# Performance work log

Measured on AMD Instinct MI355X. Metric: run time of the kernel, lower is better.

## Reference

```python
import jax, jax.numpy as jnp
import numpy as np

N = 50000      # nodes
E = 800000     # edges (before self-loops)
F_IN = 128     # node feature dim (= hidden)
HID = 128      # hidden
H = 4          # heads
C = HID // H   # per-head channels = 32
L = 4          # conv_feat + 3 GATLayers
G = 128        # graphs in batch
EPS = 1e-5
BN_BIAS = 1e-4


def setup_inputs() -> dict:
    key = jax.random.key(0)
    ks = jax.random.split(key, 12)
    s = 0.1
    x = jax.random.normal(ks[0], (N, F_IN), jnp.float32)
    edge_index = jax.random.randint(ks[1], (2, E), 0, N)
    batch = jnp.sort(jax.random.randint(ks[2], (N,), 0, G))
    gat_lin = jax.random.normal(ks[3], (L, HID, HID), jnp.float32) * s
    att_src = jax.random.normal(ks[4], (L, H, C), jnp.float32) * s
    att_dst = jax.random.normal(ks[5], (L, H, C), jnp.float32) * s
    gat_bias = jax.random.normal(ks[6], (L, HID), jnp.float32) * s
    fc_w = jax.random.normal(ks[7], (HID, HID), jnp.float32) * s
    fc_b = jax.random.normal(ks[8], (HID,), jnp.float32) * s
    cls_w = jax.random.normal(ks[9], (HID, 2), jnp.float32) * s
    cls_b = jax.random.normal(ks[10], (2,), jnp.float32) * s
    return {"x": x, "edge_index": edge_index, "batch": batch,
            "gat_lin": gat_lin, "att_src": att_src, "att_dst": att_dst,
            "gat_bias": gat_bias, "fc_w": fc_w, "fc_b": fc_b,
            "cls_w": cls_w, "cls_b": cls_b}


def batch_norm(h):
    # training-mode BN, weight=1, bias=1e-4 (per ResGAT init loop)
    m = h.mean(axis=0)
    v = h.var(axis=0)
    return (h - m) * jax.lax.rsqrt(v + EPS) + BN_BIAS


def gat_conv(x, W, a_src, a_dst, b, src, dst):
    # PyG GATConv: h = xW -> [N,H,C]; alpha_e = leaky_relu(a_src.h[src] + a_dst.h[dst]);
    # softmax over edges sharing the same dst; out[dst] += alpha * h[src]; concat heads + bias
    n = x.shape[0]
    h = (x @ W).reshape(n, H, C)
    a_s = jnp.einsum('nhc,hc->nh', h, a_src)   # [N,H]
    a_d = jnp.einsum('nhc,hc->nh', h, a_dst)   # [N,H]
    alpha = jax.nn.leaky_relu(a_s[src] + a_d[dst], 0.2)  # [E',H]
    amax = jax.lax.stop_gradient(jax.ops.segment_max(alpha, dst, num_segments=n))
    ealpha = jnp.exp(alpha - amax[dst])
    denom = jax.ops.segment_sum(ealpha, dst, num_segments=n)
    coef = ealpha / (denom[dst] + 1e-16)                 # [E',H]
    msg = h[src] * coef[:, :, None]                      # [E',H,C]
    out = jax.ops.segment_sum(msg, dst, num_segments=n)  # [N,H,C]
    return out.reshape(n, H * C) + b


def reference(x, edge_index, batch, gat_lin, att_src, att_dst, gat_bias,
              fc_w, fc_b, cls_w, cls_b):
    n = x.shape[0]
    loop = jnp.arange(n, dtype=edge_index.dtype)
    src = jnp.concatenate([edge_index[0], loop])  # add self-loops (PyG default)
    dst = jnp.concatenate([edge_index[1], loop])

    h = batch_norm(x)
    h = jax.nn.relu(gat_conv(h, gat_lin[0], att_src[0], att_dst[0], gat_bias[0], src, dst))
    for i in range(1, L):  # 3 GATLayers: relu(BN(GAT(h)) + h)
        out = gat_conv(h, gat_lin[i], att_src[i], att_dst[i], gat_bias[i], src, dst)
        h = jax.nn.relu(batch_norm(out) + h)

    g = jax.ops.segment_sum(h, batch, num_segments=G)  # global_add_pool [G,HID]
    g = jax.nn.relu(batch_norm(g) @ fc_w + fc_b)       # single FC layer (num_fc_layers=2)
    g = batch_norm(g)                                  # bn_hidden; dropout = identity (eval)
    logits = g @ cls_w + cls_b
    return jax.nn.log_softmax(logits, axis=-1)
```

## Files before the change

kernel.cpp:

```cpp
#include <hip/hip_runtime.h>
#include <math.h>

#define NF 128
#define EPS 1e-5f
#define BNB 1e-4f
#define CHUNK 8192

static inline int cdiv(int a, int b){ return (a + b - 1) / b; }

typedef __attribute__((ext_vector_type(8))) short bf16x8;
typedef __attribute__((ext_vector_type(4))) float f32x4;

__device__ __forceinline__ float lrelu(float x){ return x > 0.f ? x : 0.2f * x; }
__device__ __forceinline__ float sel4(float4 v, int h){
  float r = v.x;
  r = (h == 1) ? v.y : r;
  r = (h == 2) ? v.z : r;
  r = (h == 3) ? v.w : r;
  return r;
}

__device__ __forceinline__ unsigned short f2b(float f){
  unsigned u = __float_as_uint(f);
  u += 0x7fffu + ((u >> 16) & 1u);
  return (unsigned short)(u >> 16);
}
__device__ __forceinline__ float b2f_lo(unsigned v){ return __uint_as_float(v << 16); }
__device__ __forceinline__ float b2f_hi(unsigned v){ return __uint_as_float(v & 0xffff0000u); }

__global__ __launch_bounds__(256) void k_init(float* stats, int* bcnt, int nbkt, int statcount,
                                              const float* __restrict__ W,
                                              unsigned short* __restrict__ Wt){
  int i = blockIdx.x * blockDim.x + threadIdx.x;
  if (i < statcount) stats[i] = 0.f;
  if (i < nbkt) bcnt[i] = 0;
  int l = i >> 14, rem = i & 16383;
  int k = rem >> 7, nn = rem & 127;
  Wt[(l << 14) + nn * 128 + k] = f2b(W[i]);
}

__global__ __launch_bounds__(256) void k_bhist(const int* __restrict__ ei, int E, int n,
                                               int* __restrict__ bcnt, int nbkt){
  __shared__ int h[256];
  h[threadIdx.x] = 0;
  __syncthreads();
  int total = E + n;
  for (int i = blockIdx.x * 256 + threadIdx.x; i < total; i += gridDim.x * 256){
    int d = (i < E) ? ei[E + i] : (i - E);
    atomicAdd(&h[d >> 8], 1);
  }
  __syncthreads();
  if (threadIdx.x < nbkt && h[threadIdx.x]) atomicAdd(&bcnt[threadIdx.x], h[threadIdx.x]);
}

__global__ __launch_bounds__(256) void k_bscan(const int* __restrict__ bcnt, int* __restrict__ boff,
                                               int* __restrict__ bcursor, int nb){
  int t = threadIdx.x;
  int v = (t < nb) ? bcnt[t] : 0;
  int lane = t & 63, w = t >> 6;
  int x = v;
  #pragma unroll
  for (int d = 1; d < 64; d <<= 1){
    int y = __shfl_up(x, d, 64);
    if (lane >= d) x += y;
  }
  __shared__ int wt[4], wex[4];
  if (lane == 63) wt[w] = x;
  __syncthreads();
  if (t == 0){ int r = 0; for (int i = 0; i < 4; ++i){ wex[i] = r; r += wt[i]; } }
  __syncthreads();
  int ex = wex[w] + x - v;
  if (t < nb){ boff[t] = ex; bcursor[t] = ex; }
  if (t == nb - 1) boff[nb] = ex + v;
}

__global__ __launch_bounds__(256) void k_bscatter2(const int* __restrict__ ei, int E, int n,
                                                   int* __restrict__ bcursor,
                                                   unsigned* __restrict__ ebuf, int nbkt){
  __shared__ int h[256], base[256];
  int t = threadIdx.x;
  int total = E + n;
  int lo = blockIdx.x * CHUNK;
  int hi = min(lo + CHUNK, total);
  h[t] = 0;
  __syncthreads();
  for (int i = lo + t; i < hi; i += 256){
    int d = (i < E) ? ei[E + i] : (i - E);
    atomicAdd(&h[d >> 8], 1);
  }
  __syncthreads();
  int cnt = h[t];
  if (t < nbkt && cnt > 0) base[t] = atomicAdd(&bcursor[t], cnt);
  __syncthreads();
  h[t] = 0;
  __syncthreads();
  for (int i = lo + t; i < hi; i += 256){
    int s, d;
    if (i < E){ s = ei[i]; d = ei[E + i]; }
    else { s = i - E; d = s; }
    int b = d >> 8;
    int r = atomicAdd(&h[b], 1);
    ebuf[base[b] + r] = ((unsigned)s << 8) | (unsigned)(d & 255);
  }
}

__global__ __launch_bounds__(256) void k_bucket(const unsigned* __restrict__ ebuf,
                                                const int* __restrict__ boff,
                                                int* __restrict__ off,
                                                int* __restrict__ esrc, int n){
  __shared__ int h[256], sbase[256];
  __shared__ int wt[4], wex[4];
  int t = threadIdx.x, b = blockIdx.x;
  int lo = boff[b], hi = boff[b + 1];
  h[t] = 0;
  __syncthreads();
  for (int i = lo + t; i < hi; i += 256) atomicAdd(&h[ebuf[i] & 255u], 1);
  __syncthreads();
  int v = h[t];
  int lane = t & 63, w = t >> 6;
  int x = v;
  #pragma unroll
  for (int d = 1; d < 64; d <<= 1){
    int y = __shfl_up(x, d, 64);
    if (lane >= d) x += y;
  }
  if (lane == 63) wt[w] = x;
  __syncthreads();
  if (t == 0){ int r = 0; for (int i = 0; i < 4; ++i){ wex[i] = r; r += wt[i]; } }
  __syncthreads();
  int base = lo + wex[w] + (x - v);
  int node = b * 256 + t;
  if (node < n) off[node] = base;
  if (node == n - 1) off[n] = base + v;
  sbase[t] = base;
  __syncthreads();
  h[t] = 0;
  __syncthreads();
  for (int i = lo + t; i < hi; i += 256){
    unsigned pk = ebuf[i];
    int ld = (int)(pk & 255u);
    int s  = (int)(pk >> 8);
    int r = atomicAdd(&h[ld], 1);
    esrc[sbase[ld] + r] = s;
  }
}

__global__ __launch_bounds__(256) void k_colstats(const float* __restrict__ X, int n, float* __restrict__ out){
  __shared__ float ss[4][128], sq[4][128];
  int t = threadIdx.x, lane = t & 63, w = t >> 6;
  float sx = 0.f, sy = 0.f, qx = 0.f, qy = 0.f;
  for (int r = blockIdx.x * 4 + w; r < n; r += gridDim.x * 4){
    float2 v = *(const float2*)(X + (size_t)r * NF + lane * 2);
    sx += v.x; sy += v.y; qx += v.x * v.x; qy += v.y * v.y;
  }
  ss[w][lane * 2] = sx; ss[w][lane * 2 + 1] = sy;
  sq[w][lane * 2] = qx; sq[w][lane * 2 + 1] = qy;
  __syncthreads();
  if (t < 128){
    float tot = ss[0][t] + ss[1][t] + ss[2][t] + ss[3][t];
    atomicAdd(&out[t], tot);
  } else {
    int c = t - 128;
    float tot = sq[0][c] + sq[1][c] + sq[2][c] + sq[3][c];
    atomicAdd(&out[128 + c], tot);
  }
}

__global__ void k_bnx(const float* __restrict__ X, const float* __restrict__ stats,
                      float* __restrict__ H, ushort4* __restrict__ H16, int n){
  size_t tot4 = (size_t)n * (NF / 4);
  float inv_n = 1.f / (float)n;
  for (size_t i = blockIdx.x * (size_t)blockDim.x + threadIdx.x; i < tot4;
       i += (size_t)gridDim.x * blockDim.x){
    float4 v = ((const float4*)X)[i];
    int c0 = (int)((i * 4) % NF);
    float* vv = (float*)&v;
    #pragma unroll
    for (int j = 0; j < 4; ++j){
      float m = stats[c0 + j] * inv_n;
      float var = stats[128 + c0 + j] * inv_n - m * m;
      vv[j] = (vv[j] - m) * rsqrtf(var + EPS) + BNB;
    }
    ((float4*)H)[i] = v;
    ushort4 b;
    b.x = f2b(v.x); b.y = f2b(v.y); b.z = f2b(v.z); b.w = f2b(v.w);
    H16[i] = b;
  }
}

__global__ void k_bnres(const float* __restrict__ Xg, const float* __restrict__ stats,
                        float* __restrict__ H, ushort4* __restrict__ H16, int n){
  size_t tot4 = (size_t)n * (NF / 4);
  float inv_n = 1.f / (float)n;
  for (size_t i = blockIdx.x * (size_t)blockDim.x + threadIdx.x; i < tot4;
       i += (size_t)gridDim.x * blockDim.x){
    float4 v = ((const float4*)Xg)[i];
    float4 hc = ((const float4*)H)[i];
    int c0 = (int)((i * 4) % NF);
    float* vv = (float*)&v;
    float* hh = (float*)&hc;
    #pragma unroll
    for (int j = 0; j < 4; ++j){
      float m = stats[c0 + j] * inv_n;
      float var = stats[128 + c0 + j] * inv_n - m * m;
      float z = (vv[j] - m) * rsqrtf(var + EPS) + BNB + hh[j];
      hh[j] = fmaxf(z, 0.f);
    }
    ((float4*)H)[i] = hc;
    ushort4 b;
    b.x = f2b(hc.x); b.y = f2b(hc.y); b.z = f2b(hc.z); b.w = f2b(hc.w);
    H16[i] = b;
  }
}

__global__ __launch_bounds__(512) void k_gemm(const unsigned short* __restrict__ X,
                                              const unsigned short* __restrict__ Wt,
                                              unsigned short* __restrict__ Y,
                                              const float* __restrict__ asrc,
                                              const float* __restrict__ adst,
                                              float* __restrict__ a_s,
                                              float* __restrict__ a_d, int n){
  __shared__ unsigned short sX[128 * 128];
  __shared__ unsigned short sW[128 * 128];
  int t = threadIdx.x;
  int rbase = blockIdx.x * 128;
  #pragma unroll
  for (int i = 0; i < 4; ++i){
    int idx = t + 512 * i;
    int rn = idx >> 4, c16 = idx & 15;
    uint4 v = ((const uint4*)Wt)[idx];
    *(uint4*)&sW[rn * 128 + ((c16 ^ (rn & 7)) << 3)] = v;
  }
  #pragma unroll
  for (int i = 0; i < 4; ++i){
    int idx = t + 512 * i;
    int r = idx >> 4, c16 = idx & 15;
    int gr = rbase + r;
    uint4 v = (gr < n) ? ((const uint4*)(X + (size_t)gr * NF))[c16] : make_uint4(0, 0, 0, 0);
    *(uint4*)&sX[r * 128 + ((c16 ^ (r & 7)) << 3)] = v;
  }
  __syncthreads();
  int lane = t & 63, w = t >> 6;
  int lrow = w * 16 + (lane & 15);
  int khi = lane >> 4;
  bf16x8 a[4];
  #pragma unroll
  for (int ks = 0; ks < 4; ++ks){
    int c16 = ks * 4 + khi;
    a[ks] = *(const bf16x8*)&sX[lrow * 128 + ((c16 ^ (lrow & 7)) << 3)];
  }
  f32x4 acc[8];
  #pragma unroll
  for (int nt = 0; nt < 8; ++nt){
    f32x4 z = {0.f, 0.f, 0.f, 0.f};
    acc[nt] = z;
    int nrow = nt * 16 + (lane & 15);
    #pragma unroll
    for (int ks = 0; ks < 4; ++ks){
      int c16 = ks * 4 + khi;
      bf16x8 b = *(const bf16x8*)&sW[nrow * 128 + ((c16 ^ (nrow & 7)) << 3)];
      acc[nt] = __builtin_amdgcn_mfma_f32_16x16x32_bf16(a[ks], b, acc[nt], 0, 0, 0);
    }
  }
  #pragma unroll
  for (int nt = 0; nt < 8; ++nt){
    #pragma unroll
    for (int i = 0; i < 4; ++i){
      int r = w * 16 + (khi << 2) + i;
      int c = nt * 16 + (lane & 15);
      int csw = c ^ ((r & 7) << 3);
      sX[r * 128 + csw] = f2b(acc[nt][i]);
    }
  }
  __syncthreads();
  #pragma unroll
  for (int i = 0; i < 4; ++i){
    int idx = t + 512 * i;
    int r = idx >> 4, c16 = idx & 15;
    int gr = rbase + r;
    if (gr < n)
      ((uint4*)(Y + (size_t)gr * NF))[c16] = *(const uint4*)&sX[r * 128 + ((c16 ^ (r & 7)) << 3)];
  }
  int r = t >> 2, hh = t & 3;
  int gr = rbase + r;
  if (gr < n){
    float ps = 0.f, pd = 0.f;
    #pragma unroll
    for (int j = 0; j < 16; ++j){
      int c = hh * 32 + j * 2;
      int u = (c >> 3) ^ (r & 7);
      unsigned v = *(const unsigned*)&sX[r * 128 + (u << 3) + (c & 7)];
      float vx = b2f_lo(v), vy = b2f_hi(v);
      ps += vx * asrc[c] + vy * asrc[c + 1];
      pd += vx * adst[c] + vy * adst[c + 1];
    }
    a_s[(size_t)gr * 4 + hh] = ps;
    a_d[(size_t)gr * 4 + hh] = pd;
  }
}

__global__ __launch_bounds__(256) void k_attn(const unsigned short* __restrict__ Hm16,
                                              const float* __restrict__ a_s,
                                              const float* __restrict__ a_d,
                                              const int* __restrict__ off,
                                              const int* __restrict__ esrc,
                                              const float* __restrict__ bias,
                                              float* __restrict__ Yf,
                                              unsigned short* __restrict__ Y16,
                                              int dorelu, int n){
  int t = threadIdx.x, lane = t & 63, w = t >> 6;
  int node = blockIdx.x * 4 + w;
  if (node >= n) return;
  node = __builtin_amdgcn_readfirstlane(node);
  int head = lane >> 4;
  float4 ad4 = ((const float4*)a_d)[node];
  float adh = sel4(ad4, head);
  int lo = off[node], hi = off[node + 1];
  lo = __builtin_amdgcn_readfirstlane(lo);
  hi = __builtin_amdgcn_readfirstlane(hi);
  int fo = lane * 2;
  float sum = 0.f, ax = 0.f, ay = 0.f;
  for (int e = lo; e < hi; e += 8){
    int si[8]; float ai[8]; unsigned vi[8];
    #pragma unroll
    for (int k = 0; k < 8; ++k) si[k] = esrc[min(e + k, hi - 1)];
    #pragma unroll
    for (int k = 0; k < 8; ++k) ai[k] = a_s[(si[k] << 2) + head];
    #pragma unroll
    for (int k = 0; k < 8; ++k) vi[k] = *(const unsigned*)(Hm16 + (size_t)si[k] * NF + fo);
    #pragma unroll
    for (int k = 0; k < 8; ++k){
      float wgt = (e + k < hi) ? __expf(lrelu(ai[k] + adh)) : 0.f;
      sum += wgt;
      ax += wgt * b2f_lo(vi[k]);
      ay += wgt * b2f_hi(vi[k]);
    }
  }
  float inv = 1.f / (sum + 1e-16f);
  float2 b = *(const float2*)(bias + fo);
  float rx = ax * inv + b.x;
  float ry = ay * inv + b.y;
  if (dorelu){
    rx = fmaxf(rx, 0.f); ry = fmaxf(ry, 0.f);
    ushort2 pk; pk.x = f2b(rx); pk.y = f2b(ry);
    *(ushort2*)(Y16 + (size_t)node * NF + fo) = pk;
  }
  float2 r; r.x = rx; r.y = ry;
  *(float2*)(Yf + (size_t)node * NF + fo) = r;
}

__global__ __launch_bounds__(256) void k_pool(const float* __restrict__ H, const int* __restrict__ batch,
                                              float* __restrict__ g, int n){
  int gid = blockIdx.x;
  int t = threadIdx.x, lane = t & 63, w = t >> 6;
  int lo = 0, hi = n;
  while (lo < hi){ int mid = (lo + hi) >> 1; if (batch[mid] < gid) lo = mid + 1; else hi = mid; }
  int a = lo, b = n;
  while (a < b){ int mid = (a + b) >> 1; if (batch[mid] < gid + 1) a = mid + 1; else b = mid; }
  float sx = 0.f, sy = 0.f;
  for (int r = lo + w; r < a; r += 4){
    float2 v = *(const float2*)(H + (size_t)r * NF + lane * 2);
    sx += v.x; sy += v.y;
  }
  __shared__ float ss[4][128];
  ss[w][lane * 2] = sx; ss[w][lane * 2 + 1] = sy;
  __syncthreads();
  if (t < 128) g[(size_t)gid * NF + t] = ss[0][t] + ss[1][t] + ss[2][t] + ss[3][t];
}

__global__ __launch_bounds__(256) void k_h2(const float* __restrict__ g,
                                            const float* __restrict__ st1,
                                            const float* __restrict__ fc_w,
                                            const float* __restrict__ fc_b,
                                            float* __restrict__ hfc,
                                            float* __restrict__ st2){
  __shared__ float sA[32 * 128];
  __shared__ float sW[128 * 128];
  __shared__ float redS[8][128], redQ[8][128];
  int t = threadIdx.x;
  int rbase = blockIdx.x * 32;
  #pragma unroll
  for (int i = 0; i < 16; ++i)
    ((float4*)sW)[t + 256 * i] = ((const float4*)fc_w)[t + 256 * i];
  const float inv128 = 1.f / 128.f;
  #pragma unroll
  for (int i = 0; i < 4; ++i){
    int idx = t + 256 * i;
    int r = idx >> 5, c4 = idx & 31;
    float4 v = ((const float4*)(g + (size_t)(rbase + r) * 128))[c4];
    int c0 = c4 * 4;
    float* vv = (float*)&v;
    #pragma unroll
    for (int j = 0; j < 4; ++j){
      float m = st1[c0 + j] * inv128;
      float var = st1[128 + c0 + j] * inv128 - m * m;
      vv[j] = (vv[j] - m) * rsqrtf(var + EPS) + BNB;
    }
    ((float4*)sA)[idx] = v;
  }
  __syncthreads();
  int c0 = (t & 31) * 4, r0 = (t >> 5) * 4;
  float o[4][4];
  float4 bb = *(const float4*)(fc_b + c0);
  #pragma unroll
  for (int i = 0; i < 4; ++i){ o[i][0] = bb.x; o[i][1] = bb.y; o[i][2] = bb.z; o[i][3] = bb.w; }
  for (int k = 0; k < 128; ++k){
    float4 wv = *(const float4*)&sW[k * 128 + c0];
    #pragma unroll
    for (int i = 0; i < 4; ++i){
      float xs = sA[(r0 + i) * 128 + k];
      o[i][0] += xs * wv.x; o[i][1] += xs * wv.y;
      o[i][2] += xs * wv.z; o[i][3] += xs * wv.w;
    }
  }
  float ps[4] = {0, 0, 0, 0}, pq[4] = {0, 0, 0, 0};
  #pragma unroll
  for (int i = 0; i < 4; ++i){
    #pragma unroll
    for (int j = 0; j < 4; ++j){
      float v = fmaxf(o[i][j], 0.f);
      o[i][j] = v;
      ps[j] += v; pq[j] += v * v;
    }
    float4 wv; wv.x = o[i][0]; wv.y = o[i][1]; wv.z = o[i][2]; wv.w = o[i][3];
    *(float4*)(hfc + (size_t)(rbase + r0 + i) * 128 + c0) = wv;
  }
  int g8 = t >> 5;
  #pragma unroll
  for (int j = 0; j < 4; ++j){ redS[g8][c0 + j] = ps[j]; redQ[g8][c0 + j] = pq[j]; }
  __syncthreads();
  if (t < 128){
    float s = 0.f, q = 0.f;
    #pragma unroll
    for (int gg = 0; gg < 8; ++gg){ s += redS[gg][t]; q += redQ[gg][t]; }
    atomicAdd(&st2[t], s);
    atomicAdd(&st2[128 + t], q);
  }
}

__global__ __launch_bounds__(1024) void k_h3(const float* __restrict__ hfc,
                                             const float* __restrict__ st2,
                                             const float* __restrict__ cls_w,
                                             const float* __restrict__ cls_b,
                                             float* __restrict__ out){
  __shared__ float A[128 * 128];
  __shared__ float logits[256];
  int t = threadIdx.x;
  #pragma unroll
  for (int i = 0; i < 4; ++i)
    ((float4*)A)[t + 1024 * i] = ((const float4*)hfc)[t + 1024 * i];
  __syncthreads();
  const float inv128 = 1.f / 128.f;
  #pragma unroll
  for (int i = 0; i < 16; ++i){
    int idx = t + 1024 * i;
    int c = idx & 127;
    float m = st2[c] * inv128;
    float var = st2[128 + c] * inv128 - m * m;
    A[idx] = (A[idx] - m) * rsqrtf(var + EPS) + BNB;
  }
  __syncthreads();
  int o = t >> 2, sub = t & 3;
  int r = o >> 1, j = o & 1;
  float acc = 0.f;
  int k0 = sub * 32;
  for (int k = k0; k < k0 + 32; ++k)
    acc += A[r * 128 + k] * cls_w[k * 2 + j];
  acc += __shfl_xor(acc, 1, 64);
  acc += __shfl_xor(acc, 2, 64);
  if (sub == 0) logits[o] = acc + cls_b[j];
  __syncthreads();
  if (t < 256){
    int rr = t >> 1;
    float l0 = logits[rr * 2], l1 = logits[rr * 2 + 1];
    float mx = fmaxf(l0, l1);
    float lse = mx + logf(__expf(l0 - mx) + __expf(l1 - mx));
    out[t] = logits[t] - lse;
  }
}

extern "C" void kernel_launch(void* const* d_in, const int* in_sizes, int n_in,
                              void* d_out, int out_size, void* d_ws, size_t ws_size,
                              hipStream_t stream){
  const float* x        = (const float*)d_in[0];
  const int*   ei       = (const int*)d_in[1];
  const int*   batch    = (const int*)d_in[2];
  const float* gat_lin  = (const float*)d_in[3];
  const float* att_src  = (const float*)d_in[4];
  const float* att_dst  = (const float*)d_in[5];
  const float* gat_bias = (const float*)d_in[6];
  const float* fc_w     = (const float*)d_in[7];
  const float* fc_b     = (const float*)d_in[8];
  const float* cls_w    = (const float*)d_in[9];
  const float* cls_b    = (const float*)d_in[10];
  float* out = (float*)d_out;
  (void)n_in; (void)out_size; (void)ws_size;

  int N = in_sizes[0] / NF;
  int E = in_sizes[1] / 2;
  int total = E + N;
  int nbkt = cdiv(N, 256);

  char* p = (char*)d_ws;
  auto alloc = [&](size_t bytes) -> char* {
    char* r = p;
    p += (bytes + 255) & ~(size_t)255;
    return r;
  };
  int*   off     = (int*)alloc((size_t)(N + 1) * 4);
  int*   bcnt    = (int*)alloc((size_t)nbkt * 4);
  int*   boff    = (int*)alloc((size_t)(nbkt + 1) * 4);
  int*   bcursor = (int*)alloc((size_t)nbkt * 4);
  unsigned* ebuf = (unsigned*)alloc((size_t)total * 4);
  int*   esrc    = (int*)alloc((size_t)total * 4);
  float* stats   = (float*)alloc(8 * 256 * 4);
  float* hbuf    = (float*)alloc((size_t)N * NF * 4);
  unsigned short* hbuf16 = (unsigned short*)alloc((size_t)N * NF * 2);
  unsigned short* tmp16  = (unsigned short*)alloc((size_t)N * NF * 2);
  unsigned short* wbuf16 = (unsigned short*)alloc((size_t)4 * NF * NF * 2);
  float* gout    = (float*)alloc((size_t)N * NF * 4);
  float* a_s     = (float*)alloc((size_t)N * 4 * 4);
  float* a_d     = (float*)alloc((size_t)N * 4 * 4);
  float* gpool   = (float*)alloc(128 * NF * 4);
  float* hfc     = (float*)alloc(128 * NF * 4);

  k_init<<<256, 256, 0, stream>>>(stats, bcnt, nbkt, 1536, gat_lin, wbuf16);
  k_bhist<<<256, 256, 0, stream>>>(ei, E, N, bcnt, nbkt);
  k_bscan<<<1, 256, 0, stream>>>(bcnt, boff, bcursor, nbkt);
  k_bscatter2<<<cdiv(total, CHUNK), 256, 0, stream>>>(ei, E, N, bcursor, ebuf, nbkt);
  k_bucket<<<nbkt, 256, 0, stream>>>(ebuf, boff, off, esrc, N);

  k_colstats<<<256, 256, 0, stream>>>(x, N, stats);
  k_bnx<<<1024, 256, 0, stream>>>(x, stats, hbuf, (ushort4*)hbuf16, N);

  for (int L = 0; L < 4; ++L){
    k_gemm<<<cdiv(N, 128), 512, 0, stream>>>(hbuf16, wbuf16 + (size_t)L * NF * NF, tmp16,
                                             att_src + (size_t)L * NF, att_dst + (size_t)L * NF,
                                             a_s, a_d, N);
    if (L == 0){
      k_attn<<<cdiv(N, 4), 256, 0, stream>>>(tmp16, a_s, a_d, off, esrc,
                                             gat_bias + (size_t)L * NF,
                                             hbuf, hbuf16, 1, N);
    } else {
      k_attn<<<cdiv(N, 4), 256, 0, stream>>>(tmp16, a_s, a_d, off, esrc,
                                             gat_bias + (size_t)L * NF,
                                             gout, hbuf16, 0, N);
      k_colstats<<<256, 256, 0, stream>>>(gout, N, stats + L * 256);
      k_bnres<<<1024, 256, 0, stream>>>(gout, stats + L * 256, hbuf, (ushort4*)hbuf16, N);
    }
  }

  k_pool<<<128, 256, 0, stream>>>(hbuf, batch, gpool, N);
  k_colstats<<<32, 256, 0, stream>>>(gpool, 128, stats + 1024);
  k_h2<<<4, 256, 0, stream>>>(gpool, stats + 1024, fc_w, fc_b, hfc, stats + 1280);
  k_h3<<<1, 1024, 0, stream>>>(hfc, stats + 1280, cls_w, cls_b, out);
}
```

Measured before the change: 453.9 us.

## Fuse batch-norm and residual into GEMM prologue and pooling, use exp2

Removes the standalone BN-on-input and BN+residual+ReLU kernels. Normalization is now applied while the GEMM loads its A tile: mode 1 is plain BN, mode 2 is BN plus residual plus ReLU, and mode 2 also writes the updated fp32 residual. The final layer's BN/residual/ReLU is folded into the pooling kernel. Attention logits are prescaled by log2(e) so the edge softmax can use exp2f. This drops several full passes over the node-feature arrays, at the cost of a heavier GEMM prologue and recomputing the per-column statistics in every block.

After: 433.6 us. 1.05x faster.

```diff
diff --git a/kernel.cpp b/kernel.cpp
--- a/kernel.cpp
+++ b/kernel.cpp
@@ -5,6 +5,7 @@
 #define EPS 1e-5f
 #define BNB 1e-4f
 #define CHUNK 8192
+#define LOG2E 1.44269504088896f
 
 static inline int cdiv(int a, int b){ return (a + b - 1) / b; }
 
@@ -24,6 +25,9 @@
   unsigned u = __float_as_uint(f);
   u += 0x7fffu + ((u >> 16) & 1u);
   return (unsigned short)(u >> 16);
+}
+__device__ __forceinline__ unsigned pack2(float a, float b){
+  return (unsigned)f2b(a) | ((unsigned)f2b(b) << 16);
 }
 __device__ __forceinline__ float b2f_lo(unsigned v){ return __uint_as_float(v << 16); }
 __device__ __forceinline__ float b2f_hi(unsigned v){ return __uint_as_float(v & 0xffff0000u); }
@@ -166,54 +170,11 @@
   }
 }
 
-__global__ void k_bnx(const float* __restrict__ X, const float* __restrict__ stats,
-                      float* __restrict__ H, ushort4* __restrict__ H16, int n){
-  size_t tot4 = (size_t)n * (NF / 4);
-  float inv_n = 1.f / (float)n;
-  for (size_t i = blockIdx.x * (size_t)blockDim.x + threadIdx.x; i < tot4;
-       i += (size_t)gridDim.x * blockDim.x){
-    float4 v = ((const float4*)X)[i];
-    int c0 = (int)((i * 4) % NF);
-    float* vv = (float*)&v;
-    #pragma unroll
-    for (int j = 0; j < 4; ++j){
-      float m = stats[c0 + j] * inv_n;
-      float var = stats[128 + c0 + j] * inv_n - m * m;
-      vv[j] = (vv[j] - m) * rsqrtf(var + EPS) + BNB;
-    }
-    ((float4*)H)[i] = v;
-    ushort4 b;
-    b.x = f2b(v.x); b.y = f2b(v.y); b.z = f2b(v.z); b.w = f2b(v.w);
-    H16[i] = b;
-  }
-}
-
-__global__ void k_bnres(const float* __restrict__ Xg, const float* __restrict__ stats,
-                        float* __restrict__ H, ushort4* __restrict__ H16, int n){
-  size_t tot4 = (size_t)n * (NF / 4);
-  float inv_n = 1.f / (float)n;
-  for (size_t i = blockIdx.x * (size_t)blockDim.x + threadIdx.x; i < tot4;
-       i += (size_t)gridDim.x * blockDim.x){
-    float4 v = ((const float4*)Xg)[i];
-    float4 hc = ((const float4*)H)[i];
-    int c0 = (int)((i * 4) % NF);
-    float* vv = (float*)&v;
-    float* hh = (float*)&hc;
-    #pragma unroll
-    for (int j = 0; j < 4; ++j){
-      float m = stats[c0 + j] * inv_n;
-      float var = stats[128 + c0 + j] * inv_n - m * m;
-      float z = (vv[j] - m) * rsqrtf(var + EPS) + BNB + hh[j];
-      hh[j] = fmaxf(z, 0.f);
-    }
-    ((float4*)H)[i] = hc;
-    ushort4 b;
-    b.x = f2b(hc.x); b.y = f2b(hc.y); b.z = f2b(hc.z); b.w = f2b(hc.w);
-    H16[i] = b;
-  }
-}
-
-__global__ __launch_bounds__(512) void k_gemm(const unsigned short* __restrict__ X,
+__global__ __launch_bounds__(512) void k_gemm(const unsigned short* __restrict__ X16,
+                                              const float* __restrict__ Xa,
+                                              float* __restrict__ Xb,
+                                              const float* __restrict__ stats, float inv_n,
+                                              int mode,
                                               const unsigned short* __restrict__ Wt,
                                               unsigned short* __restrict__ Y,
                                               const float* __restrict__ asrc,
@@ -231,13 +192,66 @@
     uint4 v = ((const uint4*)Wt)[idx];
     *(uint4*)&sW[rn * 128 + ((c16 ^ (rn & 7)) << 3)] = v;
   }
-  #pragma unroll
-  for (int i = 0; i < 4; ++i){
-    int idx = t + 512 * i;
-    int r = idx >> 4, c16 = idx & 15;
-    int gr = rbase + r;
-    uint4 v = (gr < n) ? ((const uint4*)(X + (size_t)gr * NF))[c16] : make_uint4(0, 0, 0, 0);
-    *(uint4*)&sX[r * 128 + ((c16 ^ (r & 7)) << 3)] = v;
+  if (mode == 0){
+    #pragma unroll
+    for (int i = 0; i < 4; ++i){
+      int idx = t + 512 * i;
+      int r = idx >> 4, c16 = idx & 15;
+      int gr = rbase + r;
+      uint4 v = (gr < n) ? ((const uint4*)(X16 + (size_t)gr * NF))[c16] : make_uint4(0, 0, 0, 0);
+      *(uint4*)&sX[r * 128 + ((c16 ^ (r & 7)) << 3)] = v;
+    }
+  } else {
+    #pragma unroll
+    for (int i = 0; i < 4; ++i){
+      int idx = t + 512 * i;
+      int r = idx >> 4, c16 = idx & 15;
+      int gr = rbase + r;
+      int c = c16 * 8;
+      float z[8];
+      if (gr < n){
+        float4 va = *(const float4*)(Xa + (size_t)gr * NF + c);
+        float4 vb = *(const float4*)(Xa + (size_t)gr * NF + c + 4);
+        float4 m1 = *(const float4*)(stats + c);
+        float4 m2 = *(const float4*)(stats + c + 4);
+        float4 q1 = *(const float4*)(stats + 128 + c);
+        float4 q2 = *(const float4*)(stats + 128 + c + 4);
+        const float* pa = (const float*)&va; const float* pb = (const float*)&vb;
+        const float* pm1 = (const float*)&m1; const float* pm2 = (const float*)&m2;
+        const float* pq1 = (const float*)&q1; const float* pq2 = (const float*)&q2;
+        #pragma unroll
+        for (int j = 0; j < 4; ++j){
+          float m = pm1[j] * inv_n;
+          float var = pq1[j] * inv_n - m * m;
+          z[j] = (pa[j] - m) * rsqrtf(var + EPS) + BNB;
+          float m_ = pm2[j] * inv_n;
+          float var_ = pq2[j] * inv_n - m_ * m_;
+          z[4 + j] = (pb[j] - m_) * rsqrtf(var_ + EPS) + BNB;
+        }
+        if (mode == 2){
+          float4 ha = *(const float4*)(Xb + (size_t)gr * NF + c);
+          float4 hb = *(const float4*)(Xb + (size_t)gr * NF + c + 4);
+          const float* ph1 = (const float*)&ha; const float* ph2 = (const float*)&hb;
+          #pragma unroll
+          for (int j = 0; j < 4; ++j){
+            z[j]     = fmaxf(z[j]     + ph1[j], 0.f);
+            z[4 + j] = fmaxf(z[4 + j] + ph2[j], 0.f);
+          }
+          float4 o1, o2;
+          o1.x = z[0]; o1.y = z[1]; o1.z = z[2]; o1.w = z[3];
+          o2.x = z[4]; o2.y = z[5]; o2.z = z[6]; o2.w = z[7];
+          *(float4*)(Xb + (size_t)gr * NF + c) = o1;
+          *(float4*)(Xb + (size_t)gr * NF + c + 4) = o2;
+        }
+      } else {
+        #pragma unroll
+        for (int j = 0; j < 8; ++j) z[j] = 0.f;
+      }
+      uint4 u;
+      u.x = pack2(z[0], z[1]); u.y = pack2(z[2], z[3]);
+      u.z = pack2(z[4], z[5]); u.w = pack2(z[6], z[7]);
+      *(uint4*)&sX[r * 128 + ((c16 ^ (r & 7)) << 3)] = u;
+    }
   }
   __syncthreads();
   int lane = t & 63, w = t >> 6;
@@ -294,8 +308,8 @@
       ps += vx * asrc[c] + vy * asrc[c + 1];
       pd += vx * adst[c] + vy * adst[c + 1];
     }
-    a_s[(size_t)gr * 4 + hh] = ps;
-    a_d[(size_t)gr * 4 + hh] = pd;
+    a_s[(size_t)gr * 4 + hh] = ps * LOG2E;
+    a_d[(size_t)gr * 4 + hh] = pd * LOG2E;
   }
 }
 
@@ -330,7 +344,7 @@
     for (int k = 0; k < 8; ++k) vi[k] = *(const unsigned*)(Hm16 + (size_t)si[k] * NF + fo);
     #pragma unroll
     for (int k = 0; k < 8; ++k){
-      float wgt = (e + k < hi) ? __expf(lrelu(ai[k] + adh)) : 0.f;
+      float wgt = (e + k < hi) ? exp2f(lrelu(ai[k] + adh)) : 0.f;
       sum += wgt;
       ax += wgt * b2f_lo(vi[k]);
       ay += wgt * b2f_hi(vi[k]);
@@ -349,7 +363,10 @@
   *(float2*)(Yf + (size_t)node * NF + fo) = r;
 }
 
-__global__ __launch_bounds__(256) void k_pool(const float* __restrict__ H, const int* __restrict__ batch,
+__global__ __launch_bounds__(256) void k_pool(const float* __restrict__ G,
+                                              const float* __restrict__ H,
+                                              const float* __restrict__ stats, float inv_n,
+                                              const int* __restrict__ batch,
                                               float* __restrict__ g, int n){
   int gid = blockIdx.x;
   int t = threadIdx.x, lane = t & 63, w = t >> 6;
@@ -357,10 +374,17 @@
   while (lo < hi){ int mid = (lo + hi) >> 1; if (batch[mid] < gid) lo = mid + 1; else hi = mid; }
   int a = lo, b = n;
   while (a < b){ int mid = (a + b) >> 1; if (batch[mid] < gid + 1) a = mid + 1; else b = mid; }
+  int c = lane * 2;
+  float m0 = stats[c] * inv_n,     q0 = stats[128 + c] * inv_n;
+  float m1 = stats[c + 1] * inv_n, q1 = stats[128 + c + 1] * inv_n;
+  float rs0 = rsqrtf(q0 - m0 * m0 + EPS);
+  float rs1 = rsqrtf(q1 - m1 * m1 + EPS);
   float sx = 0.f, sy = 0.f;
   for (int r = lo + w; r < a; r += 4){
-    float2 v = *(const float2*)(H + (size_t)r * NF + lane * 2);
-    sx += v.x; sy += v.y;
+    float2 gv = *(const float2*)(G + (size_t)r * NF + c);
+    float2 hv = *(const float2*)(H + (size_t)r * NF + c);
+    sx += fmaxf((gv.x - m0) * rs0 + BNB + hv.x, 0.f);
+    sy += fmaxf((gv.y - m1) * rs1 + BNB + hv.y, 0.f);
   }
   __shared__ float ss[4][128];
   ss[w][lane * 2] = sx; ss[w][lane * 2 + 1] = sy;
@@ -500,6 +524,7 @@
   int E = in_sizes[1] / 2;
   int total = E + N;
   int nbkt = cdiv(N, 256);
+  float inv_n = 1.f / (float)N;
 
   char* p = (char*)d_ws;
   auto alloc = [&](size_t bytes) -> char* {
@@ -531,26 +556,30 @@
   k_bucket<<<nbkt, 256, 0, stream>>>(ebuf, boff, off, esrc, N);
 
   k_colstats<<<256, 256, 0, stream>>>(x, N, stats);
-  k_bnx<<<1024, 256, 0, stream>>>(x, stats, hbuf, (ushort4*)hbuf16, N);
 
   for (int L = 0; L < 4; ++L){
-    k_gemm<<<cdiv(N, 128), 512, 0, stream>>>(hbuf16, wbuf16 + (size_t)L * NF * NF, tmp16,
-                                             att_src + (size_t)L * NF, att_dst + (size_t)L * NF,
-                                             a_s, a_d, N);
     if (L == 0){
+      k_gemm<<<cdiv(N, 128), 512, 0, stream>>>(hbuf16, x, hbuf, stats, inv_n, 1,
+                                               wbuf16 + (size_t)L * NF * NF, tmp16,
+                                               att_src + (size_t)L * NF, att_dst + (size_t)L * NF,
+                                               a_s, a_d, N);
       k_attn<<<cdiv(N, 4), 256, 0, stream>>>(tmp16, a_s, a_d, off, esrc,
                                              gat_bias + (size_t)L * NF,
                                              hbuf, hbuf16, 1, N);
     } else {
+      int mode = (L == 1) ? 0 : 2;
+      k_gemm<<<cdiv(N, 128), 512, 0, stream>>>(hbuf16, gout, hbuf, stats + (L - 1) * 256, inv_n, mode,
+                                               wbuf16 + (size_t)L * NF * NF, tmp16,
+                                               att_src + (size_t)L * NF, att_dst + (size_t)L * NF,
+                                               a_s, a_d, N);
       k_attn<<<cdiv(N, 4), 256, 0, stream>>>(tmp16, a_s, a_d, off, esrc,
                                              gat_bias + (size_t)L * NF,
                                              gout, hbuf16, 0, N);
       k_colstats<<<256, 256, 0, stream>>>(gout, N, stats + L * 256);
-      k_bnres<<<1024, 256, 0, stream>>>(gout, stats + L * 256, hbuf, (ushort4*)hbuf16, N);
-    }
-  }
-
-  k_pool<<<128, 256, 0, stream>>>(hbuf, batch, gpool, N);
+    }
+  }
+
+  k_pool<<<128, 256, 0, stream>>>(gout, hbuf, stats + 3 * 256, inv_n, batch, gpool, N);
   k_colstats<<<32, 256, 0, stream>>>(gpool, 128, stats + 1024);
   k_h2<<<4, 256, 0, stream>>>(gpool, stats + 1024, fc_w, fc_b, hfc, stats + 1280);
   k_h3<<<1, 1024, 0, stream>>>(hfc, stats + 1280, cls_w, cls_b, out);
```
